# Performance work log

Hardware: AMD Instinct MI355X
Metric: run time of the kernel (lower is better)

Reference implementation:

```python
import jax, jax.numpy as jnp
import numpy as np

D_MODEL = 768
N_HEADS = 12
D_HEAD = D_MODEL // N_HEADS
TEMP = float(np.sqrt(D_HEAD))


def setup_inputs() -> dict:
    key = jax.random.key(0)
    ks = jax.random.split(key, 12)
    B, S, D = 8, 2048, D_MODEL
    patches = jax.random.normal(ks[0], (B, S, D), dtype=jnp.float32)
    in_weight = jax.random.uniform(ks[1], (D * 3, D), dtype=jnp.float32)
    in_bias = jax.random.uniform(ks[2], (D * 3,), dtype=jnp.float32)
    out_w = jax.random.normal(ks[3], (D, D), dtype=jnp.float32) * (1.0 / np.sqrt(D))
    out_b = jnp.zeros((D,), dtype=jnp.float32)
    mlp_w1 = jax.random.normal(ks[4], (4 * D, D), dtype=jnp.float32) * (1.0 / np.sqrt(D))
    mlp_b1 = jnp.zeros((4 * D,), dtype=jnp.float32)
    mlp_w2 = jax.random.normal(ks[5], (D, 4 * D), dtype=jnp.float32) * (1.0 / np.sqrt(4 * D))
    mlp_b2 = jnp.zeros((D,), dtype=jnp.float32)
    ln1_g = jnp.ones((D,), dtype=jnp.float32)
    ln1_b = jnp.zeros((D,), dtype=jnp.float32)
    ln2_g = jnp.ones((D,), dtype=jnp.float32)
    ln2_b = jnp.zeros((D,), dtype=jnp.float32)
    return {
        "patches": patches,
        "in_weight": in_weight, "in_bias": in_bias,
        "out_w": out_w, "out_b": out_b,
        "mlp_w1": mlp_w1, "mlp_b1": mlp_b1,
        "mlp_w2": mlp_w2, "mlp_b2": mlp_b2,
        "ln1_g": ln1_g, "ln1_b": ln1_b,
        "ln2_g": ln2_g, "ln2_b": ln2_b,
    }


def layer_norm(x, g, b, eps=1e-5):
    mu = jnp.mean(x, axis=-1, keepdims=True)
    var = jnp.var(x, axis=-1, keepdims=True)
    return (x - mu) * jax.lax.rsqrt(var + eps) * g + b


def mha(x, in_weight, in_bias, out_w, out_b):
    # Replicate quirky per-head reshape: [3D, D] -> [H, d_head, 3, D]
    W = in_weight.reshape(N_HEADS, D_HEAD, 3, D_MODEL)  # h, e, 3, d
    Bv = in_bias.reshape(N_HEADS, D_HEAD, 3)            # h, e, 3
    qw, kw, vw = W[:, :, 0, :], W[:, :, 1, :], W[:, :, 2, :]  # [H, e, D]
    qb, kb, vb = Bv[:, :, 0], Bv[:, :, 1], Bv[:, :, 2]        # [H, e]
    # Q,K,V per head: [B, H, S, e]
    Q = jnp.einsum('bsd,hed->bhse', x, qw) + qb[None, :, None, :]
    K = jnp.einsum('bsd,hed->bhse', x, kw) + kb[None, :, None, :]
    V = jnp.einsum('bsd,hed->bhse', x, vw) + vb[None, :, None, :]
    atn = jnp.einsum('bhse,bhte->bhst', Q, K)
    atn = jax.nn.softmax(atn / TEMP, axis=-1)
    # NOTE: original uses V (not atn @ V) as head output; heads concatenated over feature dim
    B_, H, S, e = V.shape
    heads = jnp.transpose(V, (0, 2, 1, 3)).reshape(B_, S, H * e)
    masks = jnp.sum(atn, axis=1)  # sum over heads: [B, S, S]
    out = heads @ out_w.T + out_b
    return out, masks


def reference(patches, in_weight, in_bias, out_w, out_b,
              mlp_w1, mlp_b1, mlp_w2, mlp_b2,
              ln1_g, ln1_b, ln2_g, ln2_b):
    x = layer_norm(patches, ln1_g, ln1_b)
    sa, _ = mha(x, in_weight, in_bias, out_w, out_b)
    x = sa + x  # dropout = identity (eval)
    x = layer_norm(x, ln2_g, ln2_b)
    h = jax.nn.selu(x @ mlp_w1.T + mlp_b1)
    x = (h @ mlp_w2.T + mlp_b2) + x
    return x
```

## Files before the change

### kernel.cpp

```cpp
#include <hip/hip_runtime.h>


typedef __bf16 bf16;
typedef __bf16 bf16x8 __attribute__((ext_vector_type(8)));
typedef __bf16 bf16x4 __attribute__((ext_vector_type(4)));
typedef float  f32x4  __attribute__((ext_vector_type(4)));

#define N_ROWS  16384

__global__ __launch_bounds__(256) void cast_kernel(const float* __restrict__ x,
                                                   bf16* __restrict__ y, int n4) {
  int i = blockIdx.x * 256 + threadIdx.x;
  if (i >= n4) return;
  float4 v = ((const float4*)x)[i];
  bf16x4 o = {(bf16)v.x, (bf16)v.y, (bf16)v.z, (bf16)v.w};
  *(bf16x4*)(y + 4 * (size_t)i) = o;
}

__global__ __launch_bounds__(256) void wvt_kernel(const float* __restrict__ in_weight,
                                                  bf16* __restrict__ wvt) {
  int k = blockIdx.x * 256 + threadIdx.x;
  int j = blockIdx.y;
  wvt[(size_t)k * 768 + j] = (bf16)in_weight[((size_t)j * 3 + 2) * 768 + k];
}

__global__ __launch_bounds__(64) void bias_combine_kernel(const float* __restrict__ out_w,
                                                          const float* __restrict__ in_bias,
                                                          const float* __restrict__ out_b,
                                                          float* __restrict__ bc) {
  int n = blockIdx.x, l = threadIdx.x;
  float s = 0.f;
  for (int j = l; j < 768; j += 64) s += out_w[(size_t)n * 768 + j] * in_bias[j * 3 + 2];
#pragma unroll
  for (int off = 32; off > 0; off >>= 1) s += __shfl_xor(s, off, 64);
  if (l == 0) bc[n] = s + out_b[n];
}

__global__ __launch_bounds__(256) void ln_kernel(const float* __restrict__ x,
                                                 const float* __restrict__ g,
                                                 const float* __restrict__ b,
                                                 bf16* __restrict__ y) {
  const int row = blockIdx.x;
  const float* xr = x + (size_t)row * 768;
  float v[3], s1 = 0.f, s2 = 0.f;
#pragma unroll
  for (int i = 0; i < 3; ++i) {
    v[i] = xr[threadIdx.x + i * 256];
    s1 += v[i];
    s2 += v[i] * v[i];
  }
#pragma unroll
  for (int off = 32; off > 0; off >>= 1) {
    s1 += __shfl_xor(s1, off, 64);
    s2 += __shfl_xor(s2, off, 64);
  }
  __shared__ float red[8];
  int w = threadIdx.x >> 6, l = threadIdx.x & 63;
  if (l == 0) { red[w * 2] = s1; red[w * 2 + 1] = s2; }
  __syncthreads();
  s1 = red[0] + red[2] + red[4] + red[6];
  s2 = red[1] + red[3] + red[5] + red[7];
  const float mu = s1 * (1.f / 768.f);
  const float var = s2 * (1.f / 768.f) - mu * mu;
  const float rstd = rsqrtf(var + 1e-5f);
#pragma unroll
  for (int i = 0; i < 3; ++i) {
    int d = threadIdx.x + i * 256;
    y[(size_t)row * 768 + d] = (bf16)((v[i] - mu) * rstd * g[d] + b[d]);
  }
}

template <int EPI>
__global__ __launch_bounds__(256) void gemm_bt(const bf16* __restrict__ A,
                                               const bf16* __restrict__ B,
                                               const float* __restrict__ bias,
                                               const bf16* __restrict__ resid,
                                               void* __restrict__ out,
                                               int M, int N, int K) {
  __shared__ bf16 sA[128 * 32];
  __shared__ bf16 sB[128 * 32];
  const int tid = threadIdx.x;
  const int w = tid >> 6, l = tid & 63;
  const int wr = w >> 1, wc = w & 1;
  const int q = l >> 4, m16 = l & 15;

  int mtile, ntile;
  {
    const int L = blockIdx.y * gridDim.x + blockIdx.x;
    const int gy = gridDim.y;
    if ((gy & 7) == 0) {
      const int mpx = gy >> 3;
      const int xcd = L & 7;
      const int slot = L >> 3;
      mtile = xcd * mpx + (slot % mpx);
      ntile = slot / mpx;
    } else {
      mtile = blockIdx.y; ntile = blockIdx.x;
    }
  }
  const long tileM = (long)mtile * 128;
  const long tileN = (long)ntile * 128;

  f32x4 acc[4][4] = {};

  for (int k0 = 0; k0 < K; k0 += 32) {
#pragma unroll
    for (int i = 0; i < 2; ++i) {
      const int ch = tid + i * 256;
      const int row = ch >> 2;
      const int clog = ((ch & 3) - (row >> 1)) & 3;
      const bf16* ga = A + (tileM + row) * (long)K + k0 + clog * 8;
      const bf16* gb = B + (tileN + row) * (long)K + k0 + clog * 8;
      __builtin_amdgcn_global_load_lds(
          (const __attribute__((address_space(1))) void*)ga,
          (__attribute__((address_space(3))) void*)(&sA[ch * 8]), 16, 0, 0);
      __builtin_amdgcn_global_load_lds(
          (const __attribute__((address_space(1))) void*)gb,
          (__attribute__((address_space(3))) void*)(&sB[ch * 8]), 16, 0, 0);
    }
    __syncthreads();

    bf16x8 af[4], bfr[4];
#pragma unroll
    for (int mi = 0; mi < 4; ++mi) {
      const int r = wr * 64 + mi * 16 + m16;
      af[mi] = *(const bf16x8*)&sA[r * 32 + (((q + (r >> 1)) & 3) << 3)];
    }
#pragma unroll
    for (int ni = 0; ni < 4; ++ni) {
      const int r = wc * 64 + ni * 16 + m16;
      bfr[ni] = *(const bf16x8*)&sB[r * 32 + (((q + (r >> 1)) & 3) << 3)];
    }
#pragma unroll
    for (int mi = 0; mi < 4; ++mi)
#pragma unroll
      for (int ni = 0; ni < 4; ++ni)
        acc[mi][ni] = __builtin_amdgcn_mfma_f32_16x16x32_bf16(af[mi], bfr[ni],
                                                              acc[mi][ni], 0, 0, 0);
    __syncthreads();
  }

  const long colBase = tileN + wc * 64 + m16;
  const long rowBase = tileM + wr * 64 + q * 4;
#pragma unroll
  for (int mi = 0; mi < 4; ++mi) {
#pragma unroll
    for (int r = 0; r < 4; ++r) {
      const long row = rowBase + mi * 16 + r;
#pragma unroll
      for (int ni = 0; ni < 4; ++ni) {
        const long col = colBase + ni * 16;
        float v = acc[mi][ni][r];
        if (EPI == 0) {
          ((bf16*)out)[row * N + col] = (bf16)v;
        } else if (EPI == 1) {
          v += bias[col] + (float)resid[row * N + col];
          ((float*)out)[row * N + col] = v;
        } else {
          v += bias[col];
          v = v > 0.f ? 1.0507009873554805f * v
                      : 1.0507009873554805f * 1.6732632423543772f * (__expf(v) - 1.f);
          ((bf16*)out)[row * N + col] = (bf16)v;
        }
      }
    }
  }
}

extern "C" void kernel_launch(void* const* d_in, const int* in_sizes, int n_in,
                              void* d_out, int out_size, void* d_ws, size_t ws_size,
                              hipStream_t stream) {
  const float* patches   = (const float*)d_in[0];
  const float* in_weight = (const float*)d_in[1];
  const float* in_bias   = (const float*)d_in[2];
  const float* out_w     = (const float*)d_in[3];
  const float* out_b     = (const float*)d_in[4];
  const float* mlp_w1    = (const float*)d_in[5];
  const float* mlp_b1    = (const float*)d_in[6];
  const float* mlp_w2    = (const float*)d_in[7];
  const float* mlp_b2    = (const float*)d_in[8];
  const float* ln1_g     = (const float*)d_in[9];
  const float* ln1_b     = (const float*)d_in[10];
  const float* ln2_g     = (const float*)d_in[11];
  const float* ln2_b     = (const float*)d_in[12];

  char* ws = (char*)d_ws;
  const size_t MB = 1024 * 1024;
  bf16* Wc   = (bf16*)(ws + 0);
  bf16* w1b  = (bf16*)(ws + 2 * MB);
  bf16* w2b  = (bf16*)(ws + 8 * MB);
  bf16* owb  = (bf16*)(ws + 14 * MB);
  bf16* wvt  = (bf16*)(ws + 16 * MB);
  float* bc  = (float*)(ws + 18 * MB);
  bf16* X1   = (bf16*)(ws + 20 * MB);
  bf16* X3   = (bf16*)(ws + 20 * MB);
  bf16* H    = (bf16*)(ws + 48 * MB);
  float* X2  = (float*)d_out;

  cast_kernel<<<(3072 * 768 / 4 + 255) / 256, 256, 0, stream>>>(mlp_w1, w1b, 3072 * 768 / 4);
  cast_kernel<<<(768 * 3072 / 4 + 255) / 256, 256, 0, stream>>>(mlp_w2, w2b, 768 * 3072 / 4);
  cast_kernel<<<(768 * 768 / 4 + 255) / 256, 256, 0, stream>>>(out_w, owb, 768 * 768 / 4);
  wvt_kernel<<<dim3(3, 768), 256, 0, stream>>>(in_weight, wvt);
  bias_combine_kernel<<<768, 64, 0, stream>>>(out_w, in_bias, out_b, bc);
  gemm_bt<0><<<dim3(6, 6), 256, 0, stream>>>(owb, wvt, nullptr, nullptr, Wc, 768, 768, 768);

  ln_kernel<<<N_ROWS, 256, 0, stream>>>(patches, ln1_g, ln1_b, X1);
  gemm_bt<1><<<dim3(6, 128), 256, 0, stream>>>(X1, Wc, bc, X1, X2, N_ROWS, 768, 768);
  ln_kernel<<<N_ROWS, 256, 0, stream>>>(X2, ln2_g, ln2_b, X3);
  gemm_bt<2><<<dim3(24, 128), 256, 0, stream>>>(X3, w1b, mlp_b1, nullptr, H, N_ROWS, 3072, 768);
  gemm_bt<1><<<dim3(6, 128), 256, 0, stream>>>(H, w2b, mlp_b2, X3, d_out, N_ROWS, 768, 3072);
}
```

Before: 476.2 us.

## Pipeline GEMM with 4-slot LDS ring, widen tiles, fuse casts, bf16 intermediate

The GEMM now uses 512-thread blocks with 128x256 tiles and a 4-slot LDS ring buffer. Global-to-LDS loads run three K-steps ahead, gated by explicit vmcnt waits and a single barrier per step, so load latency overlaps MFMA work. The three weight-cast launches are merged into one kernel, and the V-weight transpose now goes through a shared-memory tile. The post-attention intermediate is stored as bf16 rather than fp32, so the second layernorm reads half the bytes, at some cost in precision. Larger tiles with fewer blocks per grid may lower occupancy or tail efficiency on the narrow N=768 GEMMs.

```diff
diff --git a/kernel.cpp b/kernel.cpp
--- a/kernel.cpp
+++ b/kernel.cpp
@@ -8,20 +8,42 @@
 
 #define N_ROWS  16384
 
-__global__ __launch_bounds__(256) void cast_kernel(const float* __restrict__ x,
-                                                   bf16* __restrict__ y, int n4) {
+#define AS1(p) ((const __attribute__((address_space(1))) void*)(p))
+#define AS3(p) ((__attribute__((address_space(3))) void*)(p))
+
+#define VM6 0x0F76
+#define VM3 0x0F73
+#define VM0 0x0F70
+
+#define N1 589824
+#define N2 589824
+#define N3 147456
+__global__ __launch_bounds__(256) void prep_cast(const float* __restrict__ w1,
+                                                 const float* __restrict__ w2,
+                                                 const float* __restrict__ ow,
+                                                 bf16* __restrict__ w1b,
+                                                 bf16* __restrict__ w2b,
+                                                 bf16* __restrict__ owb) {
   int i = blockIdx.x * 256 + threadIdx.x;
-  if (i >= n4) return;
-  float4 v = ((const float4*)x)[i];
+  const float* src; bf16* dst; int off;
+  if (i < N1)           { src = w1; dst = w1b; off = i; }
+  else if (i < N1 + N2) { src = w2; dst = w2b; off = i - N1; }
+  else                  { src = ow; dst = owb; off = i - N1 - N2; }
+  float4 v = ((const float4*)src)[off];
   bf16x4 o = {(bf16)v.x, (bf16)v.y, (bf16)v.z, (bf16)v.w};
-  *(bf16x4*)(y + 4 * (size_t)i) = o;
+  *(bf16x4*)(dst + 4 * (size_t)off) = o;
 }
 
 __global__ __launch_bounds__(256) void wvt_kernel(const float* __restrict__ in_weight,
                                                   bf16* __restrict__ wvt) {
-  int k = blockIdx.x * 256 + threadIdx.x;
-  int j = blockIdx.y;
-  wvt[(size_t)k * 768 + j] = (bf16)in_weight[((size_t)j * 3 + 2) * 768 + k];
+  __shared__ float t[64][65];
+  const int k0 = blockIdx.x * 64, j0 = blockIdx.y * 64;
+  const int tx = threadIdx.x & 63, ty = threadIdx.x >> 6;
+  for (int jj = ty; jj < 64; jj += 4)
+    t[jj][tx] = in_weight[((size_t)(j0 + jj) * 3 + 2) * 768 + k0 + tx];
+  __syncthreads();
+  for (int kk = ty; kk < 64; kk += 4)
+    wvt[(size_t)(k0 + kk) * 768 + j0 + tx] = (bf16)t[tx][kk];
 }
 
 __global__ __launch_bounds__(64) void bias_combine_kernel(const float* __restrict__ out_w,
@@ -36,16 +58,17 @@
   if (l == 0) bc[n] = s + out_b[n];
 }
 
-__global__ __launch_bounds__(256) void ln_kernel(const float* __restrict__ x,
+template <typename TIN>
+__global__ __launch_bounds__(256) void ln_kernel(const TIN* __restrict__ x,
                                                  const float* __restrict__ g,
                                                  const float* __restrict__ b,
                                                  bf16* __restrict__ y) {
   const int row = blockIdx.x;
-  const float* xr = x + (size_t)row * 768;
+  const TIN* xr = x + (size_t)row * 768;
   float v[3], s1 = 0.f, s2 = 0.f;
 #pragma unroll
   for (int i = 0; i < 3; ++i) {
-    v[i] = xr[threadIdx.x + i * 256];
+    v[i] = (float)xr[threadIdx.x + i * 256];
     s1 += v[i];
     s2 += v[i] * v[i];
   }
@@ -70,18 +93,18 @@
   }
 }
 
+#define SLOT_E (384 * 32)
 template <int EPI>
-__global__ __launch_bounds__(256) void gemm_bt(const bf16* __restrict__ A,
-                                               const bf16* __restrict__ B,
-                                               const float* __restrict__ bias,
-                                               const bf16* __restrict__ resid,
-                                               void* __restrict__ out,
-                                               int M, int N, int K) {
-  __shared__ bf16 sA[128 * 32];
-  __shared__ bf16 sB[128 * 32];
+__global__ __launch_bounds__(512, 2) void gemm_bt(const bf16* __restrict__ A,
+                                                  const bf16* __restrict__ B,
+                                                  const float* __restrict__ bias,
+                                                  const bf16* __restrict__ resid,
+                                                  void* __restrict__ out,
+                                                  int M, int N, int K) {
+  __shared__ bf16 ring[4 * SLOT_E];
   const int tid = threadIdx.x;
   const int w = tid >> 6, l = tid & 63;
-  const int wr = w >> 1, wc = w & 1;
+  const int wr = w >> 2, wcn = w & 3;
   const int q = l >> 4, m16 = l & 15;
 
   int mtile, ntile;
@@ -99,49 +122,85 @@
     }
   }
   const long tileM = (long)mtile * 128;
-  const long tileN = (long)ntile * 128;
+  const long tileN = (long)ntile * 256;
+
+  const int rowA = tid >> 2;
+  const int clA = ((tid & 3) - (rowA >> 1)) & 3;
+  const bf16* gA = A + (tileM + rowA) * (long)K + clA * 8;
+  const int ldA = tid * 8;
+  const bf16* gB[2]; int ldB[2];
+#pragma unroll
+  for (int j = 0; j < 2; ++j) {
+    const int ch = tid + j * 512;
+    const int row = ch >> 2;
+    const int cl = ((ch & 3) - (row >> 1)) & 3;
+    gB[j] = B + (tileN + row) * (long)K + cl * 8;
+    ldB[j] = ch * 8;
+  }
+
+  int offA[4], offB[4];
+#pragma unroll
+  for (int mi = 0; mi < 4; ++mi) {
+    const int r = wr * 64 + mi * 16 + m16;
+    offA[mi] = r * 32 + (((q + (r >> 1)) & 3) << 3);
+  }
+#pragma unroll
+  for (int ni = 0; ni < 4; ++ni) {
+    const int r = wcn * 64 + ni * 16 + m16;
+    offB[ni] = r * 32 + (((q + (r >> 1)) & 3) << 3);
+  }
 
   f32x4 acc[4][4] = {};
 
-  for (int k0 = 0; k0 < K; k0 += 32) {
-#pragma unroll
-    for (int i = 0; i < 2; ++i) {
-      const int ch = tid + i * 256;
-      const int row = ch >> 2;
-      const int clog = ((ch & 3) - (row >> 1)) & 3;
-      const bf16* ga = A + (tileM + row) * (long)K + k0 + clog * 8;
-      const bf16* gb = B + (tileN + row) * (long)K + k0 + clog * 8;
-      __builtin_amdgcn_global_load_lds(
-          (const __attribute__((address_space(1))) void*)ga,
-          (__attribute__((address_space(3))) void*)(&sA[ch * 8]), 16, 0, 0);
-      __builtin_amdgcn_global_load_lds(
-          (const __attribute__((address_space(1))) void*)gb,
-          (__attribute__((address_space(3))) void*)(&sB[ch * 8]), 16, 0, 0);
-    }
-    __syncthreads();
-
-    bf16x8 af[4], bfr[4];
-#pragma unroll
-    for (int mi = 0; mi < 4; ++mi) {
-      const int r = wr * 64 + mi * 16 + m16;
-      af[mi] = *(const bf16x8*)&sA[r * 32 + (((q + (r >> 1)) & 3) << 3)];
-    }
-#pragma unroll
-    for (int ni = 0; ni < 4; ++ni) {
-      const int r = wc * 64 + ni * 16 + m16;
-      bfr[ni] = *(const bf16x8*)&sB[r * 32 + (((q + (r >> 1)) & 3) << 3)];
-    }
-#pragma unroll
-    for (int mi = 0; mi < 4; ++mi)
-#pragma unroll
-      for (int ni = 0; ni < 4; ++ni)
-        acc[mi][ni] = __builtin_amdgcn_mfma_f32_16x16x32_bf16(af[mi], bfr[ni],
-                                                              acc[mi][ni], 0, 0, 0);
-    __syncthreads();
-  }
-
-  const long colBase = tileN + wc * 64 + m16;
-  const long rowBase = tileM + wr * 64 + q * 4;
+#pragma unroll
+  for (int s = 0; s < 3; ++s) {
+    bf16* da = ring + s * SLOT_E;
+    bf16* db = da + 128 * 32;
+    __builtin_amdgcn_global_load_lds(AS1(gA + s * 32), AS3(&da[ldA]), 16, 0, 0);
+#pragma unroll
+    for (int j = 0; j < 2; ++j)
+      __builtin_amdgcn_global_load_lds(AS1(gB[j] + s * 32), AS3(&db[ldB[j]]), 16, 0, 0);
+  }
+  long k_next = 96;
+
+#define KSTEP(SLOT, WIMM, ISSUE)                                               \
+  {                                                                            \
+    __builtin_amdgcn_s_waitcnt(WIMM);                                          \
+    __builtin_amdgcn_s_barrier();                                              \
+    if (ISSUE) {                                                               \
+      bf16* da = ring + (((SLOT) + 3) & 3) * SLOT_E;                           \
+      bf16* db = da + 128 * 32;                                                \
+      __builtin_amdgcn_global_load_lds(AS1(gA + k_next), AS3(&da[ldA]), 16, 0, 0); \
+      _Pragma("unroll")                                                        \
+      for (int j = 0; j < 2; ++j)                                              \
+        __builtin_amdgcn_global_load_lds(AS1(gB[j] + k_next), AS3(&db[ldB[j]]), 16, 0, 0); \
+      k_next += 32;                                                            \
+    }                                                                          \
+    const bf16* ca = ring + (SLOT) * SLOT_E;                                   \
+    const bf16* cb = ca + 128 * 32;                                            \
+    bf16x8 bfr[4];                                                             \
+    _Pragma("unroll")                                                          \
+    for (int ni = 0; ni < 4; ++ni) bfr[ni] = *(const bf16x8*)&cb[offB[ni]];    \
+    _Pragma("unroll")                                                          \
+    for (int mi = 0; mi < 4; ++mi) {                                           \
+      const bf16x8 af = *(const bf16x8*)&ca[offA[mi]];                         \
+      _Pragma("unroll")                                                        \
+      for (int ni = 0; ni < 4; ++ni)                                           \
+        acc[mi][ni] = __builtin_amdgcn_mfma_f32_16x16x32_bf16(af, bfr[ni],     \
+                                                              acc[mi][ni], 0, 0, 0); \
+    }                                                                          \
+  }
+
+  const int T = K >> 5;
+#pragma unroll 1
+  for (int g = 0; g < T - 4; g += 4) {
+    KSTEP(0, VM6, 1) KSTEP(1, VM6, 1) KSTEP(2, VM6, 1) KSTEP(3, VM6, 1)
+  }
+  KSTEP(0, VM6, 1) KSTEP(1, VM6, 0) KSTEP(2, VM3, 0) KSTEP(3, VM0, 0)
+#undef KSTEP
+
+  const long colBase = tileN + (long)wcn * 64 + m16;
+  const long rowBase = tileM + (long)wr * 64 + q * 4;
 #pragma unroll
   for (int mi = 0; mi < 4; ++mi) {
 #pragma unroll
@@ -156,10 +215,13 @@
         } else if (EPI == 1) {
           v += bias[col] + (float)resid[row * N + col];
           ((float*)out)[row * N + col] = v;
-        } else {
+        } else if (EPI == 2) {
           v += bias[col];
           v = v > 0.f ? 1.0507009873554805f * v
                       : 1.0507009873554805f * 1.6732632423543772f * (__expf(v) - 1.f);
+          ((bf16*)out)[row * N + col] = (bf16)v;
+        } else {
+          v += bias[col] + (float)resid[row * N + col];
           ((bf16*)out)[row * N + col] = (bf16)v;
         }
       }
@@ -194,19 +256,18 @@
   float* bc  = (float*)(ws + 18 * MB);
   bf16* X1   = (bf16*)(ws + 20 * MB);
   bf16* X3   = (bf16*)(ws + 20 * MB);
+  bf16* X2b  = (bf16*)(ws + 48 * MB);
   bf16* H    = (bf16*)(ws + 48 * MB);
-  float* X2  = (float*)d_out;
-
-  cast_kernel<<<(3072 * 768 / 4 + 255) / 256, 256, 0, stream>>>(mlp_w1, w1b, 3072 * 768 / 4);
-  cast_kernel<<<(768 * 3072 / 4 + 255) / 256, 256, 0, stream>>>(mlp_w2, w2b, 768 * 3072 / 4);
-  cast_kernel<<<(768 * 768 / 4 + 255) / 256, 256, 0, stream>>>(out_w, owb, 768 * 768 / 4);
-  wvt_kernel<<<dim3(3, 768), 256, 0, stream>>>(in_weight, wvt);
+
+  prep_cast<<<(N1 + N2 + N3) / 256, 256, 0, stream>>>(mlp_w1, mlp_w2, out_w,
+                                                      w1b, w2b, owb);
+  wvt_kernel<<<dim3(12, 12), 256, 0, stream>>>(in_weight, wvt);
   bias_combine_kernel<<<768, 64, 0, stream>>>(out_w, in_bias, out_b, bc);
-  gemm_bt<0><<<dim3(6, 6), 256, 0, stream>>>(owb, wvt, nullptr, nullptr, Wc, 768, 768, 768);
-
-  ln_kernel<<<N_ROWS, 256, 0, stream>>>(patches, ln1_g, ln1_b, X1);
-  gemm_bt<1><<<dim3(6, 128), 256, 0, stream>>>(X1, Wc, bc, X1, X2, N_ROWS, 768, 768);
-  ln_kernel<<<N_ROWS, 256, 0, stream>>>(X2, ln2_g, ln2_b, X3);
-  gemm_bt<2><<<dim3(24, 128), 256, 0, stream>>>(X3, w1b, mlp_b1, nullptr, H, N_ROWS, 3072, 768);
-  gemm_bt<1><<<dim3(6, 128), 256, 0, stream>>>(H, w2b, mlp_b2, X3, d_out, N_ROWS, 768, 3072);
-}
+  gemm_bt<0><<<dim3(3, 6), 512, 0, stream>>>(owb, wvt, nullptr, nullptr, Wc, 768, 768, 768);
+
+  ln_kernel<float><<<N_ROWS, 256, 0, stream>>>(patches, ln1_g, ln1_b, X1);
+  gemm_bt<3><<<dim3(3, 128), 512, 0, stream>>>(X1, Wc, bc, X1, X2b, N_ROWS, 768, 768);
+  ln_kernel<bf16><<<N_ROWS, 256, 0, stream>>>(X2b, ln2_g, ln2_b, X3);
+  gemm_bt<2><<<dim3(12, 128), 512, 0, stream>>>(X3, w1b, mlp_b1, nullptr, H, N_ROWS, 3072, 768);
+  gemm_bt<1><<<dim3(3, 128), 512, 0, stream>>>(H, w2b, mlp_b2, X3, d_out, N_ROWS, 768, 3072);
+}
```

New measurement: 407.6 us. -14.4%, faster.
